# Kernel tuning notes

Hardware: AMD Instinct MI355X
Metric: run time of the kernel (lower is better)

## Reference

```python
import itertools
import jax, jax.numpy as jnp
import numpy as np

N_QUBITS = 8
N_LAYERS = 2
BATCH = 8192
INPUT_DIM = 3072
NUM_CLASSES = 10

_In = np.eye(2, dtype=np.complex64)
_Xn = np.array([[0, 1], [1, 0]], dtype=np.complex64)
_Yn = np.array([[0, -1j], [1j, 0]], dtype=np.complex64)
_Zn = np.array([[1, 0], [0, -1]], dtype=np.complex64)
_P = {"I": _In, "X": _Xn, "Y": _Yn, "Z": _Zn}
_XX = jnp.asarray(np.kron(_Xn, _Xn))
_YY = jnp.asarray(np.kron(_Yn, _Yn))
_ZZ = jnp.asarray(np.kron(_Zn, _Zn))
_I4 = jnp.eye(4, dtype=jnp.complex64)
# 2-qubit Pauli words in PennyLane ArbitraryUnitary order: IX, IY, IZ, XI, ..., ZZ
_WORDS = jnp.asarray(np.stack([np.kron(_P[a], _P[b]) for a, b in itertools.product("IXYZ", repeat=2)][1:]))


def apply_gate(state, U, wires):
    """Apply a 2^k x 2^k gate U to the given wires of a (2,)*n statevector."""
    n = state.ndim
    k = len(wires)
    U = U.reshape((2,) * (2 * k)).astype(state.dtype)
    state = jnp.tensordot(U, state, axes=(list(range(k, 2 * k)), list(wires)))
    rest = [a for a in range(n) if a not in wires]
    perm = [0] * n
    for i, a in enumerate(wires):
        perm[a] = i
    for j, a in enumerate(rest):
        perm[a] = k + j
    return jnp.transpose(state, perm)


def u3_mat(t, p, d):
    ct, st = jnp.cos(t / 2).astype(jnp.complex64), jnp.sin(t / 2).astype(jnp.complex64)
    r0 = jnp.stack([ct, -jnp.exp(1j * d) * st])
    r1 = jnp.stack([jnp.exp(1j * p) * st, jnp.exp(1j * (p + d)) * ct])
    return jnp.stack([r0, r1])


def ry_mat(t):
    c, s = jnp.cos(t / 2), jnp.sin(t / 2)
    return jnp.stack([jnp.stack([c, -s]), jnp.stack([s, c])]).astype(jnp.complex64)


def ising_mat(phi, pauli2):
    # exp(-i phi/2 P) for two-qubit Pauli word P (P^2 = I)
    return jnp.cos(phi / 2) * _I4 - 1j * jnp.sin(phi / 2) * pauli2


def circuit(conv_w, pool_w, last_w, feats):
    state = jnp.zeros((2,) * N_QUBITS, jnp.complex64).at[(0,) * N_QUBITS].set(1.0)
    # AngleEmbedding with RY rotations
    for w in range(N_QUBITS):
        state = apply_gate(state, ry_mat(feats[w]), (w,))
    wires = list(range(N_QUBITS))
    for layer in range(N_LAYERS):
        cw = conv_w[layer]
        nw = len(wires)
        for p in (0, 1):
            for idx in range(nw - 1):
                if idx % 2 == p:
                    a, b = wires[idx], wires[idx + 1]
                    state = apply_gate(state, u3_mat(cw[idx, 0], cw[idx, 1], cw[idx, 2]), (a,))
                    state = apply_gate(state, u3_mat(cw[idx + 1, 3], cw[idx + 1, 4], cw[idx + 1, 5]), (b,))
                    state = apply_gate(state, ising_mat(cw[idx, 6], _ZZ), (a, b))
                    state = apply_gate(state, ising_mat(cw[idx, 7], _YY), (a, b))
                    state = apply_gate(state, ising_mat(cw[idx, 8], _XX), (a, b))
                    state = apply_gate(state, u3_mat(cw[idx, 9], cw[idx, 10], cw[idx, 11]), (a,))
                    state = apply_gate(state, u3_mat(cw[idx + 1, 12], cw[idx + 1, 13], cw[idx + 1, 14]), (b,))
        # Pooling: mid-circuit measure + conditional U3 == (deferred measurement)
        pw = pool_w[layer]
        for idx in range(1, nw, 2):
            u = u3_mat(pw[idx // 2, 0], pw[idx // 2, 1], pw[idx // 2, 2])
            cu = jnp.zeros((4, 4), jnp.complex64).at[0, 0].set(1.0).at[1, 1].set(1.0).at[2:, 2:].set(u)
            state = apply_gate(state, cu, (wires[idx], wires[idx - 1]))
        wires = wires[::2]
    # ArbitraryUnitary on remaining 2 wires: product of 15 PauliRot gates
    for k in range(15):
        mat = jnp.cos(last_w[k] / 2) * _I4 - 1j * jnp.sin(last_w[k] / 2) * _WORDS[k]
        state = apply_gate(state, mat, tuple(wires))
    probs = state.real ** 2 + state.imag ** 2
    z = jnp.sum(probs, axis=tuple(range(1, N_QUBITS)))  # (2,)
    return z[0] - z[1]


def setup_inputs() -> dict:
    key = jax.random.key(0)
    ks = jax.random.split(key, 8)
    return {
        "x": jax.random.normal(ks[0], (BATCH, INPUT_DIM), jnp.float32),
        "fc_w": jax.random.normal(ks[1], (N_QUBITS, INPUT_DIM), jnp.float32) * 0.02,
        "fc_b": jnp.zeros((N_QUBITS,), jnp.float32),
        "conv_params": jax.random.normal(ks[2], (N_LAYERS, N_QUBITS, 15), jnp.float32),
        "pool_params": jax.random.normal(ks[3], (N_LAYERS, N_QUBITS // 2, 3), jnp.float32),
        "last_params": jax.random.normal(ks[4], (15,), jnp.float32),
        "out_w": jax.random.normal(ks[5], (NUM_CLASSES, 1), jnp.float32),
        "out_b": jnp.zeros((NUM_CLASSES,), jnp.float32),
    }


def reference(x, fc_w, fc_b, conv_params, pool_params, last_params, out_w, out_b):
    feats = jnp.tanh(x.reshape(x.shape[0], -1) @ fc_w.T + fc_b)  # (B, n_qubits)
    qvals = jax.vmap(lambda f: circuit(conv_params, pool_params, last_params, f))(feats)
    logits = qvals[:, None].astype(x.dtype) @ out_w.T + out_b  # (B, num_classes)
    return logits
```

## Files before the change

### kernel.cpp

```cpp
#include <hip/hip_runtime.h>
#include <math.h>

__constant__ int G_ORD[17] = {0,1,2,3,4,5,6, 10,11,12,13, 7,8,9, 14,15, 16};
__constant__ int G_WA[17]  = {0,2,4,6,1,3,5, 1,3,5,7, 0,4,2, 2,6, 0};
__constant__ int G_WB[17]  = {1,3,5,7,2,4,6, 0,2,4,6, 2,6,4, 0,4, 4};
__constant__ int CDESC[10][3] = {{0,0,1},{0,2,3},{0,4,5},{0,6,7},{0,1,2},{0,3,4},{0,5,6},
                                 {1,0,1},{1,2,3},{1,1,2}};
__constant__ int PDESC[6][2] = {{0,0},{0,1},{0,2},{0,3},{1,0},{1,1}};
__constant__ float2 PMAT[4][4] = {
  {{1.f,0.f},{0.f,0.f},{0.f,0.f},{1.f,0.f}},
  {{0.f,0.f},{1.f,0.f},{1.f,0.f},{0.f,0.f}},
  {{0.f,0.f},{0.f,-1.f},{0.f,1.f},{0.f,0.f}},
  {{1.f,0.f},{0.f,0.f},{0.f,0.f},{-1.f,0.f}}};

__device__ __forceinline__ float2 cmul(float2 a, float2 b){
  return make_float2(a.x*b.x - a.y*b.y, a.x*b.y + a.y*b.x);
}
__device__ __forceinline__ float2 cadd(float2 a, float2 b){
  return make_float2(a.x+b.x, a.y+b.y);
}
__device__ __forceinline__ float rl(float v, int l){
  return __int_as_float(__builtin_amdgcn_readlane(__float_as_int(v), l));
}

__device__ void u3m(float t, float p, float d, float2* u){
  float ct = cosf(0.5f*t), st = sinf(0.5f*t);
  u[0] = make_float2(ct, 0.f);
  u[1] = make_float2(-cosf(d)*st, -sinf(d)*st);
  u[2] = make_float2(cosf(p)*st,  sinf(p)*st);
  u[3] = make_float2(cosf(p+d)*ct, sinf(p+d)*ct);
}

__device__ void kron2(const float2* A, const float2* B, float2* M){
  #pragma unroll
  for (int ia=0; ia<2; ia++)
    #pragma unroll
    for (int ib=0; ib<2; ib++)
      #pragma unroll
      for (int ja=0; ja<2; ja++)
        #pragma unroll
        for (int jb=0; jb<2; jb++)
          M[(ia*2+ib)*4 + (ja*2+jb)] = cmul(A[ia*2+ja], B[ib*2+jb]);
}

__device__ void mul44(const float2* A, const float2* B, float2* C){
  #pragma unroll
  for (int r=0;r<4;r++)
    #pragma unroll
    for (int c=0;c<4;c++){
      float2 s = make_float2(0.f,0.f);
      #pragma unroll
      for (int k=0;k<4;k++) s = cadd(s, cmul(A[r*4+k], B[k*4+c]));
      C[r*4+c] = s;
    }
}

__device__ void rotword(float phi, int qa, int qb, float2* R){
  float ch = cosf(0.5f*phi), sh = sinf(0.5f*phi);
  float2 W[16];
  kron2(PMAT[qa], PMAT[qb], W);
  #pragma unroll
  for (int i=0;i<16;i++) R[i] = make_float2(sh*W[i].y, -sh*W[i].x);
  #pragma unroll
  for (int d=0;d<4;d++) R[d*4+d].x += ch;
}

__global__ __launch_bounds__(64) void build_u_kernel(
    const float* __restrict__ conv, const float* __restrict__ pool,
    const float* __restrict__ last, float2* __restrict__ U){
  __shared__ float2 gl[17][16];
  __shared__ float2 st[256];
  int t = threadIdx.x, col = blockIdx.x;
  {
    float2 M[16], T[16], R[16];
    if (t < 10){
      int layer = CDESC[t][0], ra = CDESC[t][1], rb = CDESC[t][2];
      const float* cw = conv + layer*120;
      int bA = ra*15, bB = rb*15;
      float2 A1[4], B1[4], A2[4], B2[4], K[16];
      u3m(cw[bA+0], cw[bA+1], cw[bA+2], A1);
      u3m(cw[bB+3], cw[bB+4], cw[bB+5], B1);
      kron2(A1, B1, M);
      rotword(cw[bA+6], 3, 3, R); mul44(R, M, T);
      rotword(cw[bA+7], 2, 2, R); mul44(R, T, M);
      rotword(cw[bA+8], 1, 1, R); mul44(R, M, T);
      u3m(cw[bA+9],  cw[bA+10], cw[bA+11], A2);
      u3m(cw[bB+12], cw[bB+13], cw[bB+14], B2);
      kron2(A2, B2, K); mul44(K, T, M);
    } else if (t < 16){
      int layer = PDESC[t-10][0], h = PDESC[t-10][1];
      const float* pw = pool + layer*12 + h*3;
      float2 u[4];
      u3m(pw[0], pw[1], pw[2], u);
      #pragma unroll
      for (int i=0;i<16;i++) M[i] = make_float2(0.f,0.f);
      M[0]  = make_float2(1.f,0.f);
      M[5]  = make_float2(1.f,0.f);
      M[10] = u[0]; M[11] = u[1]; M[14] = u[2]; M[15] = u[3];
    } else if (t == 16){
      #pragma unroll
      for (int i=0;i<16;i++) M[i] = make_float2((i%5==0)?1.f:0.f, 0.f);
      for (int k=0;k<15;k++){
        int w = k+1;
        rotword(last[k], w>>2, w&3, R);
        mul44(R, M, T);
        #pragma unroll
        for (int i=0;i<16;i++) M[i] = T[i];
      }
    }
    if (t < 17){
      #pragma unroll
      for (int i=0;i<16;i++) gl[t][i] = M[i];
    }
  }
  #pragma unroll
  for (int k=t; k<256; k+=64) st[k] = make_float2(k==col ? 1.f : 0.f, 0.f);
  __syncthreads();
  for (int g=0; g<17; g++){
    int slot = G_ORD[g];
    float2 m[16];
    #pragma unroll
    for (int i=0;i<16;i++) m[i] = gl[slot][i];
    int pa = 7 - G_WA[g], pb = 7 - G_WB[g];
    int plo = pa < pb ? pa : pb, phi_ = pa < pb ? pb : pa;
    int mm = t;
    int t1   = ((mm >> plo) << (plo+1)) | (mm & ((1<<plo)-1));
    int base = ((t1 >> phi_) << (phi_+1)) | (t1 & ((1<<phi_)-1));
    int ba = 1<<pa, bb = 1<<pb;
    int i0 = base, i1 = base|bb, i2 = base|ba, i3 = base|ba|bb;
    float2 s0 = st[i0], s1 = st[i1], s2 = st[i2], s3 = st[i3];
    float2 n0 = cadd(cadd(cmul(m[0], s0), cmul(m[1], s1)), cadd(cmul(m[2], s2), cmul(m[3], s3)));
    float2 n1 = cadd(cadd(cmul(m[4], s0), cmul(m[5], s1)), cadd(cmul(m[6], s2), cmul(m[7], s3)));
    float2 n2 = cadd(cadd(cmul(m[8], s0), cmul(m[9], s1)), cadd(cmul(m[10],s2), cmul(m[11],s3)));
    float2 n3 = cadd(cadd(cmul(m[12],s0), cmul(m[13],s1)), cadd(cmul(m[14],s2), cmul(m[15],s3)));
    st[i0] = n0; st[i1] = n1; st[i2] = n2; st[i3] = n3;
    __syncthreads();
  }
  #pragma unroll
  for (int k=t; k<256; k+=64) U[k*256 + col] = st[k];
}

__global__ __launch_bounds__(256) void build_a_kernel(
    const float2* __restrict__ U, float* __restrict__ A){
  int j = threadIdx.x, i0 = blockIdx.x*2;
  float a0=0.f, a1=0.f;
  #pragma unroll 8
  for (int k=0; k<256; k++){
    float2 uj = U[k*256 + j];
    float2 u0 = U[k*256 + i0+0];
    float2 u1 = U[k*256 + i0+1];
    float sgn = (k < 128) ? 1.f : -1.f;
    a0 += sgn*(u0.x*uj.x + u0.y*uj.y);
    a1 += sgn*(u1.x*uj.x + u1.y*uj.y);
  }
  A[(i0+0)*256 + j] = a0;
  A[(i0+1)*256 + j] = a1;
}

__global__ __launch_bounds__(256, 4) void main_kernel(
    const float* __restrict__ x, const float* __restrict__ fcw,
    const float* __restrict__ fcb, const float* __restrict__ Ag,
    const float* __restrict__ outw, const float* __restrict__ outb,
    float* __restrict__ out){
  __shared__ float lds[4352];
  __shared__ float flds[64];
  __shared__ float qpart[4][8];
  float* red = lds;
  float* ps  = lds;
  int t = threadIdx.x, lane = t & 63, wv = t >> 6, jb = lane;
  int r0 = blockIdx.x * 8;
  {
    int rw = r0 + wv*2;
    const float4* x4 = (const float4*)x;
    const float4* w4 = (const float4*)fcw;
    float acc[2][8];
    #pragma unroll
    for (int r=0;r<2;r++)
      #pragma unroll
      for (int o=0;o<8;o++) acc[r][o] = 0.f;
    #pragma unroll 2
    for (int p=0; p<12; p++){
      float4 wf[8];
      #pragma unroll
      for (int o=0;o<8;o++) wf[o] = w4[o*768 + p*64 + lane];
      #pragma unroll
      for (int r=0;r<2;r++){
        float4 xv = x4[(size_t)(rw+r)*768 + p*64 + lane];
        #pragma unroll
        for (int o=0;o<8;o++){
          acc[r][o] += xv.x*wf[o].x + xv.y*wf[o].y + xv.z*wf[o].z + xv.w*wf[o].w;
        }
      }
    }
    #pragma unroll
    for (int r=0;r<2;r++)
      #pragma unroll
      for (int o=0;o<8;o++)
        red[((wv*2+r)*8 + o)*68 + lane] = acc[r][o];
  }
  __syncthreads();
  if (t < 64){
    const float4* rp = (const float4*)(red + t*68);
    float4 s4 = make_float4(0.f,0.f,0.f,0.f);
    #pragma unroll
    for (int i=0;i<16;i++){
      float4 v = rp[i];
      s4.x += v.x; s4.y += v.y; s4.z += v.z; s4.w += v.w;
    }
    flds[t] = tanhf(s4.x + s4.y + s4.z + s4.w + fcb[t & 7]);
  }
  __syncthreads();
  {
    int row = t >> 5, idx = t & 31, i1 = idx & 15, jh = idx >> 4;
    const float* f = flds + row*8;
    float c[8], s[8];
    #pragma unroll
    for (int w=0; w<8; w++){
      float a = 0.5f*f[w];
      __sincosf(a, &s[w], &c[w]);
    }
    float Hv = (i1&8 ? s[0]:c[0]) * (i1&4 ? s[1]:c[1])
             * (i1&2 ? s[2]:c[2]) * (i1&1 ? s[3]:c[3]);
    float l2[2], l4[4], l8[8], L[16];
    l2[0]=c[4]; l2[1]=s[4];
    #pragma unroll
    for (int a=0;a<2;a++){ l4[a*2]=l2[a]*c[5]; l4[a*2+1]=l2[a]*s[5]; }
    #pragma unroll
    for (int a=0;a<4;a++){ l8[a*2]=l4[a]*c[6]; l8[a*2+1]=l4[a]*s[6]; }
    #pragma unroll
    for (int a=0;a<8;a++){ L[a*2]=l8[a]*c[7]; L[a*2+1]=l8[a]*s[7]; }
    float4* dst = (float4*)(ps + row*256 + i1*16 + jh*8);
    #pragma unroll
    for (int qd=0; qd<2; qd++){
      int b = jh*8 + qd*4;
      dst[qd] = make_float4(Hv*L[b+0], Hv*L[b+1], Hv*L[b+2], Hv*L[b+3]);
    }
  }
  __syncthreads();
  float psiK[8];
  #pragma unroll
  for (int r=0; r<8; r++) psiK[r] = ps[r*256 + wv*64 + lane];
  const float4* Ag4 = (const float4*)Ag;
  float4 acc4[8];
  #pragma unroll
  for (int r=0;r<8;r++) acc4[r] = make_float4(0.f,0.f,0.f,0.f);
  #pragma unroll 2
  for (int g=0; g<16; g++){
    int k0 = wv*64 + g*4;
    float4 a0 = Ag4[(size_t)(k0+0)*64 + jb];
    float4 a1 = Ag4[(size_t)(k0+1)*64 + jb];
    float4 a2 = Ag4[(size_t)(k0+2)*64 + jb];
    float4 a3 = Ag4[(size_t)(k0+3)*64 + jb];
    int l0 = g*4;
    #pragma unroll
    for (int r=0; r<8; r++){
      float p0 = rl(psiK[r], l0+0);
      float p1 = rl(psiK[r], l0+1);
      float p2 = rl(psiK[r], l0+2);
      float p3 = rl(psiK[r], l0+3);
      acc4[r].x += p0*a0.x + p1*a1.x + p2*a2.x + p3*a3.x;
      acc4[r].y += p0*a0.y + p1*a1.y + p2*a2.y + p3*a3.y;
      acc4[r].z += p0*a0.z + p1*a1.z + p2*a2.z + p3*a3.z;
      acc4[r].w += p0*a0.w + p1*a1.w + p2*a2.w + p3*a3.w;
    }
  }
  const float4* ps4 = (const float4*)ps;
  #pragma unroll
  for (int r=0; r<8; r++){
    float4 pc = ps4[r*64 + jb];
    float q = acc4[r].x*pc.x + acc4[r].y*pc.y + acc4[r].z*pc.z + acc4[r].w*pc.w;
    #pragma unroll
    for (int m=1; m<64; m<<=1) q += __shfl_xor(q, m, 64);
    if (lane == 0) qpart[wv][r] = q;
  }
  __syncthreads();
  if (t < 80){
    int row = t / 10, c = t - row*10;
    float q = qpart[0][row] + qpart[1][row] + qpart[2][row] + qpart[3][row];
    out[(r0 + row)*10 + c] = q*outw[c] + outb[c];
  }
}

extern "C" void kernel_launch(void* const* d_in, const int* in_sizes, int n_in,
                              void* d_out, int out_size, void* d_ws, size_t ws_size,
                              hipStream_t stream) {
  const float* x    = (const float*)d_in[0];
  const float* fcw  = (const float*)d_in[1];
  const float* fcb  = (const float*)d_in[2];
  const float* conv = (const float*)d_in[3];
  const float* pool = (const float*)d_in[4];
  const float* last = (const float*)d_in[5];
  const float* outw = (const float*)d_in[6];
  const float* outb = (const float*)d_in[7];
  float* out = (float*)d_out;

  float* ws = (float*)d_ws;
  float2* U  = (float2*)ws;
  float*  Am = ws + 131072;

  build_u_kernel<<<256, 64, 0, stream>>>(conv, pool, last, U);
  build_a_kernel<<<128, 256, 0, stream>>>(U, Am);
  main_kernel<<<1024, 256, 0, stream>>>(x, fcw, fcb, Am, outw, outb, out);
}
```

Measured before the change: 246.5 us.

## Split fused main kernel into separate feature-projection and quadratic-form kernels

```diff
diff --git a/kernel.cpp b/kernel.cpp
--- a/kernel.cpp
+++ b/kernel.cpp
@@ -157,62 +157,62 @@
   A[(i0+1)*256 + j] = a1;
 }
 
-__global__ __launch_bounds__(256, 4) void main_kernel(
+__global__ __launch_bounds__(256) void feats_kernel(
     const float* __restrict__ x, const float* __restrict__ fcw,
-    const float* __restrict__ fcb, const float* __restrict__ Ag,
+    const float* __restrict__ fcb, float* __restrict__ feats){
+  __shared__ float part[4][32];
+  int t = threadIdx.x, lane = t & 63, wv = t >> 6;
+  int r0 = blockIdx.x * 4;
+  const float4* x4 = (const float4*)x;
+  const float4* w4 = (const float4*)fcw;
+  float acc[32];
+  #pragma unroll
+  for (int i=0;i<32;i++) acc[i] = 0.f;
+  int kb = wv*192;
+  #pragma unroll
+  for (int p=0; p<3; p++){
+    float4 wf[8];
+    #pragma unroll
+    for (int o=0;o<8;o++) wf[o] = w4[o*768 + kb + p*64 + lane];
+    #pragma unroll
+    for (int r=0;r<4;r++){
+      float4 xv = x4[(size_t)(r0+r)*768 + kb + p*64 + lane];
+      #pragma unroll
+      for (int o=0;o<8;o++)
+        acc[r*8+o] += xv.x*wf[o].x + xv.y*wf[o].y + xv.z*wf[o].z + xv.w*wf[o].w;
+    }
+  }
+  #pragma unroll
+  for (int i=0;i<32;i++) acc[i] += __shfl_xor(acc[i], 32, 64);
+  #pragma unroll
+  for (int o=16; o>=1; o>>=1){
+    #pragma unroll
+    for (int i=0; i<o; i++){
+      float a = acc[i], b = acc[i+o];
+      float sel = (lane & o) ? a : b;
+      float tt  = __shfl_xor(sel, o, 64);
+      acc[i] = ((lane & o) ? b : a) + tt;
+    }
+  }
+  if (lane < 32) part[wv][lane] = acc[0];
+  __syncthreads();
+  if (t < 32){
+    float s = part[0][t] + part[1][t] + part[2][t] + part[3][t] + fcb[t & 7];
+    feats[(r0 + (t>>3))*8 + (t&7)] = tanhf(s);
+  }
+}
+
+__global__ __launch_bounds__(256, 4) void qform_kernel(
+    const float* __restrict__ Ag, const float* __restrict__ feats,
     const float* __restrict__ outw, const float* __restrict__ outb,
     float* __restrict__ out){
-  __shared__ float lds[4352];
-  __shared__ float flds[64];
+  __shared__ float ps[2048];
   __shared__ float qpart[4][8];
-  float* red = lds;
-  float* ps  = lds;
   int t = threadIdx.x, lane = t & 63, wv = t >> 6, jb = lane;
   int r0 = blockIdx.x * 8;
   {
-    int rw = r0 + wv*2;
-    const float4* x4 = (const float4*)x;
-    const float4* w4 = (const float4*)fcw;
-    float acc[2][8];
-    #pragma unroll
-    for (int r=0;r<2;r++)
-      #pragma unroll
-      for (int o=0;o<8;o++) acc[r][o] = 0.f;
-    #pragma unroll 2
-    for (int p=0; p<12; p++){
-      float4 wf[8];
-      #pragma unroll
-      for (int o=0;o<8;o++) wf[o] = w4[o*768 + p*64 + lane];
-      #pragma unroll
-      for (int r=0;r<2;r++){
-        float4 xv = x4[(size_t)(rw+r)*768 + p*64 + lane];
-        #pragma unroll
-        for (int o=0;o<8;o++){
-          acc[r][o] += xv.x*wf[o].x + xv.y*wf[o].y + xv.z*wf[o].z + xv.w*wf[o].w;
-        }
-      }
-    }
-    #pragma unroll
-    for (int r=0;r<2;r++)
-      #pragma unroll
-      for (int o=0;o<8;o++)
-        red[((wv*2+r)*8 + o)*68 + lane] = acc[r][o];
-  }
-  __syncthreads();
-  if (t < 64){
-    const float4* rp = (const float4*)(red + t*68);
-    float4 s4 = make_float4(0.f,0.f,0.f,0.f);
-    #pragma unroll
-    for (int i=0;i<16;i++){
-      float4 v = rp[i];
-      s4.x += v.x; s4.y += v.y; s4.z += v.z; s4.w += v.w;
-    }
-    flds[t] = tanhf(s4.x + s4.y + s4.z + s4.w + fcb[t & 7]);
-  }
-  __syncthreads();
-  {
     int row = t >> 5, idx = t & 31, i1 = idx & 15, jh = idx >> 4;
-    const float* f = flds + row*8;
+    const float* f = feats + (r0 + row)*8;
     float c[8], s[8];
     #pragma unroll
     for (int w=0; w<8; w++){
@@ -295,10 +295,12 @@
   float* out = (float*)d_out;
 
   float* ws = (float*)d_ws;
-  float2* U  = (float2*)ws;
-  float*  Am = ws + 131072;
+  float2* U     = (float2*)ws;
+  float*  Am    = ws + 131072;
+  float*  feats = Am + 65536;
 
   build_u_kernel<<<256, 64, 0, stream>>>(conv, pool, last, U);
   build_a_kernel<<<128, 256, 0, stream>>>(U, Am);
-  main_kernel<<<1024, 256, 0, stream>>>(x, fcw, fcb, Am, outw, outb, out);
-}
+  feats_kernel<<<2048, 256, 0, stream>>>(x, fcw, fcb, feats);
+  qform_kernel<<<1024, 256, 0, stream>>>(Am, feats, outw, outb, out);
+}
```

Result: slower. 285.6 us (+15.9%).

## Split feature projection from quadratic-form kernel and precompute gates once

Applied to the files above, without the earlier changes.

```diff
diff --git a/kernel.cpp b/kernel.cpp
--- a/kernel.cpp
+++ b/kernel.cpp
@@ -65,65 +65,69 @@
   for (int d=0;d<4;d++) R[d*4+d].x += ch;
 }
 
+__global__ __launch_bounds__(64) void build_gates_kernel(
+    const float* __restrict__ conv, const float* __restrict__ pool,
+    const float* __restrict__ last, float* __restrict__ gates){
+  int t = threadIdx.x;
+  float2 M[16], T[16], R[16];
+  if (t < 10){
+    int layer = CDESC[t][0], ra = CDESC[t][1], rb = CDESC[t][2];
+    const float* cw = conv + layer*120;
+    int bA = ra*15, bB = rb*15;
+    float2 A1[4], B1[4], A2[4], B2[4], K[16];
+    u3m(cw[bA+0], cw[bA+1], cw[bA+2], A1);
+    u3m(cw[bB+3], cw[bB+4], cw[bB+5], B1);
+    kron2(A1, B1, M);
+    rotword(cw[bA+6], 3, 3, R); mul44(R, M, T);
+    rotword(cw[bA+7], 2, 2, R); mul44(R, T, M);
+    rotword(cw[bA+8], 1, 1, R); mul44(R, M, T);
+    u3m(cw[bA+9],  cw[bA+10], cw[bA+11], A2);
+    u3m(cw[bB+12], cw[bB+13], cw[bB+14], B2);
+    kron2(A2, B2, K); mul44(K, T, M);
+  } else if (t < 16){
+    int layer = PDESC[t-10][0], h = PDESC[t-10][1];
+    const float* pw = pool + layer*12 + h*3;
+    float2 u[4];
+    u3m(pw[0], pw[1], pw[2], u);
+    #pragma unroll
+    for (int i=0;i<16;i++) M[i] = make_float2(0.f,0.f);
+    M[0]  = make_float2(1.f,0.f);
+    M[5]  = make_float2(1.f,0.f);
+    M[10] = u[0]; M[11] = u[1]; M[14] = u[2]; M[15] = u[3];
+  } else if (t == 16){
+    #pragma unroll
+    for (int i=0;i<16;i++) M[i] = make_float2((i%5==0)?1.f:0.f, 0.f);
+    for (int k=0;k<15;k++){
+      int w = k+1;
+      rotword(last[k], w>>2, w&3, R);
+      mul44(R, M, T);
+      #pragma unroll
+      for (int i=0;i<16;i++) M[i] = T[i];
+    }
+  }
+  if (t < 17){
+    float2* dst = (float2*)(gates + t*32);
+    #pragma unroll
+    for (int i=0;i<16;i++) dst[i] = M[i];
+  }
+}
+
 __global__ __launch_bounds__(64) void build_u_kernel(
-    const float* __restrict__ conv, const float* __restrict__ pool,
-    const float* __restrict__ last, float2* __restrict__ U){
-  __shared__ float2 gl[17][16];
+    const float* __restrict__ gates, float2* __restrict__ U){
   __shared__ float2 st[256];
-  int t = threadIdx.x, col = blockIdx.x;
-  {
-    float2 M[16], T[16], R[16];
-    if (t < 10){
-      int layer = CDESC[t][0], ra = CDESC[t][1], rb = CDESC[t][2];
-      const float* cw = conv + layer*120;
-      int bA = ra*15, bB = rb*15;
-      float2 A1[4], B1[4], A2[4], B2[4], K[16];
-      u3m(cw[bA+0], cw[bA+1], cw[bA+2], A1);
-      u3m(cw[bB+3], cw[bB+4], cw[bB+5], B1);
-      kron2(A1, B1, M);
-      rotword(cw[bA+6], 3, 3, R); mul44(R, M, T);
-      rotword(cw[bA+7], 2, 2, R); mul44(R, T, M);
-      rotword(cw[bA+8], 1, 1, R); mul44(R, M, T);
-      u3m(cw[bA+9],  cw[bA+10], cw[bA+11], A2);
-      u3m(cw[bB+12], cw[bB+13], cw[bB+14], B2);
-      kron2(A2, B2, K); mul44(K, T, M);
-    } else if (t < 16){
-      int layer = PDESC[t-10][0], h = PDESC[t-10][1];
-      const float* pw = pool + layer*12 + h*3;
-      float2 u[4];
-      u3m(pw[0], pw[1], pw[2], u);
-      #pragma unroll
-      for (int i=0;i<16;i++) M[i] = make_float2(0.f,0.f);
-      M[0]  = make_float2(1.f,0.f);
-      M[5]  = make_float2(1.f,0.f);
-      M[10] = u[0]; M[11] = u[1]; M[14] = u[2]; M[15] = u[3];
-    } else if (t == 16){
-      #pragma unroll
-      for (int i=0;i<16;i++) M[i] = make_float2((i%5==0)?1.f:0.f, 0.f);
-      for (int k=0;k<15;k++){
-        int w = k+1;
-        rotword(last[k], w>>2, w&3, R);
-        mul44(R, M, T);
-        #pragma unroll
-        for (int i=0;i<16;i++) M[i] = T[i];
-      }
-    }
-    if (t < 17){
-      #pragma unroll
-      for (int i=0;i<16;i++) gl[t][i] = M[i];
-    }
-  }
-  #pragma unroll
-  for (int k=t; k<256; k+=64) st[k] = make_float2(k==col ? 1.f : 0.f, 0.f);
+  int lane = threadIdx.x, col = blockIdx.x;
+  #pragma unroll
+  for (int k=lane; k<256; k+=64) st[k] = make_float2(k==col ? 1.f : 0.f, 0.f);
   __syncthreads();
   for (int g=0; g<17; g++){
     int slot = G_ORD[g];
+    const float2* gm = (const float2*)(gates + slot*32);
     float2 m[16];
     #pragma unroll
-    for (int i=0;i<16;i++) m[i] = gl[slot][i];
+    for (int i=0;i<16;i++) m[i] = gm[i];
     int pa = 7 - G_WA[g], pb = 7 - G_WB[g];
     int plo = pa < pb ? pa : pb, phi_ = pa < pb ? pb : pa;
-    int mm = t;
+    int mm = lane;
     int t1   = ((mm >> plo) << (plo+1)) | (mm & ((1<<plo)-1));
     int base = ((t1 >> phi_) << (phi_+1)) | (t1 & ((1<<phi_)-1));
     int ba = 1<<pa, bb = 1<<pb;
@@ -137,7 +141,7 @@
     __syncthreads();
   }
   #pragma unroll
-  for (int k=t; k<256; k+=64) U[k*256 + col] = st[k];
+  for (int k=lane; k<256; k+=64) U[k*256 + col] = st[k];
 }
 
 __global__ __launch_bounds__(256) void build_a_kernel(
@@ -157,62 +161,64 @@
   A[(i0+1)*256 + j] = a1;
 }
 
-__global__ __launch_bounds__(256, 4) void main_kernel(
+__global__ __launch_bounds__(256) void feats_kernel(
     const float* __restrict__ x, const float* __restrict__ fcw,
-    const float* __restrict__ fcb, const float* __restrict__ Ag,
+    const float* __restrict__ fcb, float* __restrict__ feats){
+  __shared__ float red[128*68];
+  int t = threadIdx.x, lane = t & 63, wv = t >> 6;
+  int r0 = blockIdx.x * 16;
+  int rw = r0 + wv*4;
+  const float4* x4 = (const float4*)x;
+  const float4* w4 = (const float4*)fcw;
+  float acc[4][8];
+  #pragma unroll
+  for (int r=0;r<4;r++)
+    #pragma unroll
+    for (int o=0;o<8;o++) acc[r][o] = 0.f;
+  #pragma unroll 2
+  for (int p=0; p<12; p++){
+    float4 wf[8];
+    #pragma unroll
+    for (int o=0;o<8;o++) wf[o] = w4[o*768 + p*64 + lane];
+    #pragma unroll
+    for (int r=0;r<4;r++){
+      float4 xv = x4[(size_t)(rw+r)*768 + p*64 + lane];
+      #pragma unroll
+      for (int o=0;o<8;o++){
+        acc[r][o] += xv.x*wf[o].x + xv.y*wf[o].y + xv.z*wf[o].z + xv.w*wf[o].w;
+      }
+    }
+  }
+  #pragma unroll
+  for (int r=0;r<4;r++)
+    #pragma unroll
+    for (int o=0;o<8;o++)
+      red[((wv*4+r)*8 + o)*68 + lane] = acc[r][o];
+  __syncthreads();
+  if (t < 128){
+    const float4* rp = (const float4*)(red + t*68);
+    float4 s4 = make_float4(0.f,0.f,0.f,0.f);
+    #pragma unroll
+    for (int i=0;i<16;i++){
+      float4 v = rp[i];
+      s4.x += v.x; s4.y += v.y; s4.z += v.z; s4.w += v.w;
+    }
+    float s = s4.x + s4.y + s4.z + s4.w + fcb[t & 7];
+    feats[(r0 + (t>>3))*8 + (t&7)] = tanhf(s);
+  }
+}
+
+__global__ __launch_bounds__(256, 4) void qform_kernel(
+    const float* __restrict__ Ag, const float* __restrict__ feats,
     const float* __restrict__ outw, const float* __restrict__ outb,
     float* __restrict__ out){
-  __shared__ float lds[4352];
-  __shared__ float flds[64];
+  __shared__ float ps[2048];
   __shared__ float qpart[4][8];
-  float* red = lds;
-  float* ps  = lds;
   int t = threadIdx.x, lane = t & 63, wv = t >> 6, jb = lane;
   int r0 = blockIdx.x * 8;
   {
-    int rw = r0 + wv*2;
-    const float4* x4 = (const float4*)x;
-    const float4* w4 = (const float4*)fcw;
-    float acc[2][8];
-    #pragma unroll
-    for (int r=0;r<2;r++)
-      #pragma unroll
-      for (int o=0;o<8;o++) acc[r][o] = 0.f;
-    #pragma unroll 2
-    for (int p=0; p<12; p++){
-      float4 wf[8];
-      #pragma unroll
-      for (int o=0;o<8;o++) wf[o] = w4[o*768 + p*64 + lane];
-      #pragma unroll
-      for (int r=0;r<2;r++){
-        float4 xv = x4[(size_t)(rw+r)*768 + p*64 + lane];
-        #pragma unroll
-        for (int o=0;o<8;o++){
-          acc[r][o] += xv.x*wf[o].x + xv.y*wf[o].y + xv.z*wf[o].z + xv.w*wf[o].w;
-        }
-      }
-    }
-    #pragma unroll
-    for (int r=0;r<2;r++)
-      #pragma unroll
-      for (int o=0;o<8;o++)
-        red[((wv*2+r)*8 + o)*68 + lane] = acc[r][o];
-  }
-  __syncthreads();
-  if (t < 64){
-    const float4* rp = (const float4*)(red + t*68);
-    float4 s4 = make_float4(0.f,0.f,0.f,0.f);
-    #pragma unroll
-    for (int i=0;i<16;i++){
-      float4 v = rp[i];
-      s4.x += v.x; s4.y += v.y; s4.z += v.z; s4.w += v.w;
-    }
-    flds[t] = tanhf(s4.x + s4.y + s4.z + s4.w + fcb[t & 7]);
-  }
-  __syncthreads();
-  {
     int row = t >> 5, idx = t & 31, i1 = idx & 15, jh = idx >> 4;
-    const float* f = flds + row*8;
+    const float* f = feats + (r0 + row)*8;
     float c[8], s[8];
     #pragma unroll
     for (int w=0; w<8; w++){
@@ -295,10 +301,17 @@
   float* out = (float*)d_out;
 
   float* ws = (float*)d_ws;
-  float2* U  = (float2*)ws;
-  float*  Am = ws + 131072;
-
-  build_u_kernel<<<256, 64, 0, stream>>>(conv, pool, last, U);
+  float*  gates = ws;
+  float2* U     = (float2*)(ws + 1024);
+  float*  Am    = ws + 1024 + 131072*2 - 131072;
+  float*  feats = ws + 1024 + 131072 + 65536;
+
+  Am    = ws + 1024 + 262144;
+  feats = Am + 65536;
+
+  feats_kernel<<<512, 256, 0, stream>>>(x, fcw, fcb, feats);
+  build_gates_kernel<<<1, 64, 0, stream>>>(conv, pool, last, gates);
+  build_u_kernel<<<256, 64, 0, stream>>>(gates, U);
   build_a_kernel<<<128, 256, 0, stream>>>(U, Am);
-  main_kernel<<<1024, 256, 0, stream>>>(x, fcw, fcb, Am, outw, outb, out);
-}
+  qform_kernel<<<1024, 256, 0, stream>>>(Am, feats, outw, outb, out);
+}
```

Measured after the change: 307.1 us. 1.25x slower.
